# Performance work log

Measured on AMD Instinct MI355X. Metric: run time of the kernel, lower is better.

Reference implementation:

```python
import jax, jax.numpy as jnp
import numpy as np

C = 128
N_SRC = 50000
N_MID = 50000
N_DST = 50000
E1 = 640000
E2 = 640000


def setup_inputs() -> dict:
    key = jax.random.key(0)
    ks = jax.random.split(key, 16)
    def lin(k):
        kw, kb = jax.random.split(k)
        bound = 1.0 / np.sqrt(C)
        W = jax.random.uniform(kw, (C, C), jnp.float32, -bound, bound)
        b = jax.random.uniform(kb, (C,), jnp.float32, -bound, bound)
        return W, b
    W1_w, W1_b = lin(ks[0])
    W2_w, W2_b = lin(ks[1])
    q_w, q_b = lin(ks[2])
    k_w, k_b = lin(ks[3])
    v_w, v_b = lin(ks[4])
    return {
        'x_src': jax.random.normal(ks[5], (N_SRC, C), jnp.float32),
        'x_mid': jax.random.normal(ks[6], (N_MID, C), jnp.float32),
        'x_dst': jax.random.normal(ks[7], (N_DST, C), jnp.float32),
        'edge_index_1': jax.random.randint(ks[8], (2, E1), 0, N_MID, jnp.int64),
        'edge_index_2': jax.random.randint(ks[9], (2, E2), 0, N_DST, jnp.int64),
        'W1_w': W1_w, 'W1_b': W1_b,
        'W2_w': W2_w, 'W2_b': W2_b,
        'q_w': q_w, 'q_b': q_b,
        'k_w': k_w, 'k_b': k_b,
        'v_w': v_w, 'v_b': v_b,
    }


def reference(x_src, x_mid, x_dst, edge_index_1, edge_index_2,
              W1_w, W1_b, W2_w, W2_b, q_w, q_b, k_w, k_b, v_w, v_b):
    src_idx_1, mid_idx_1 = edge_index_1[0], edge_index_1[1]
    # gather + small per-edge linear fuse: [E1, C]
    h_fuse = (x_mid[mid_idx_1] @ W1_w.T + W1_b) + (x_src[src_idx_1] @ W2_w.T + W2_b)
    # scatter-add into mid nodes: [N_mid, C]
    h_mid_agg = jax.ops.segment_sum(h_fuse, mid_idx_1, num_segments=x_mid.shape[0])
    mid_idx_2, dst_idx_2 = edge_index_2[0], edge_index_2[1]
    h_mid_g = h_mid_agg[mid_idx_2]          # [E2, C]
    k = h_mid_g @ k_w.T + k_b               # [E2, C]
    v = h_mid_g @ v_w.T + v_b               # [E2, C]
    q = x_dst[dst_idx_2] @ q_w.T + q_b      # [E2, C]
    scale = jnp.float32(C) ** 0.5
    # NOTE: faithful to the original: softmax is GLOBAL over all edges (dim=0)
    alpha = jax.nn.softmax((q * k).sum(-1) / scale, axis=0)  # [E2]
    msg = v * alpha[:, None]
    msg_dst = jax.ops.segment_sum(msg, dst_idx_2, num_segments=x_dst.shape[0])
    return msg_dst
```

## Files before the change

### kernel.cpp

```cpp
#include <hip/hip_runtime.h>
#include <cstdint>
#include <cstddef>


using f16   = _Float16;
using f16x2 = __attribute__((ext_vector_type(2))) _Float16;
using f16x4 = __attribute__((ext_vector_type(4))) _Float16;
using f16x8 = __attribute__((ext_vector_type(8))) _Float16;
using f32x4 = __attribute__((ext_vector_type(4))) float;

#define SP_CHUNK 2048

__device__ __forceinline__ int swzv(int v) { return v ^ ((v >> 4) & 7); }

__global__ __launch_bounds__(256) void conv_weights(
    const float* __restrict__ W1, const float* __restrict__ W2,
    const float* __restrict__ vw, const float* __restrict__ b1,
    const float* __restrict__ b2, f16* __restrict__ wh,
    float* __restrict__ b12)
{
    int idx = blockIdx.x * 256 + threadIdx.x;
    if (idx < 3 * 16384) {
        const float* src = (idx < 16384) ? W1 :
                           (idx < 2 * 16384) ? W2 : vw;
        wh[idx] = (f16)src[idx & 16383];
    } else if (idx < 3 * 16384 + 128) {
        int j = idx - 3 * 16384;
        b12[j] = b1[j] + b2[j];
    }
}

__global__ __launch_bounds__(256) void prep_qk(
    const float* __restrict__ qw, const float* __restrict__ kw,
    const float* __restrict__ qb, const float* __restrict__ kb,
    f16* __restrict__ wqk, float* __restrict__ bqk,
    float* __restrict__ wqkb, float* __restrict__ cconst)
{
    int e = blockIdx.x * 256 + threadIdx.x;
    int col = e >> 7, i = e & 127;
    float s = 0.f;
    for (int j = 0; j < 128; ++j)
        s += qw[j * 128 + i] * kw[j * 128 + col];
    wqk[col * 128 + i] = (f16)s;
    if (blockIdx.x == 0) {
        int t = threadIdx.x;
        if (t < 128) {
            float s1 = 0.f, s2 = 0.f;
            for (int j = 0; j < 128; ++j) {
                s1 += qw[j * 128 + t] * kb[j];
                s2 += qb[j] * kw[j * 128 + t];
            }
            wqkb[t] = s1;
            bqk[t] = s2;
        } else if (t == 128) {
            float s3 = 0.f;
            for (int j = 0; j < 128; ++j) s3 += qb[j] * kb[j];
            cconst[0] = s3;
        }
    }
}

__global__ __launch_bounds__(256) void conv3_f16(
    const float* __restrict__ xa, f16* __restrict__ ya, int na4,
    const float* __restrict__ xb, f16* __restrict__ yb, int nb4,
    const float* __restrict__ xc, f16* __restrict__ yc, int nc4)
{
    int j = blockIdx.x * 256 + threadIdx.x;
    const float* x; f16* y;
    if (j < na4) { x = xa; y = ya; }
    else {
        j -= na4;
        if (j < nb4) { x = xb; y = yb; }
        else {
            j -= nb4;
            if (j >= nc4) return;
            x = xc; y = yc;
        }
    }
    float4 v = ((const float4*)x)[j];
    f16x4 o = {(f16)v.x, (f16)v.y, (f16)v.z, (f16)v.w};
    ((f16x4*)y)[j] = o;
}

__global__ __launch_bounds__(256) void coarse_hist(
    const int* __restrict__ k1, int E1, int nb1, int* __restrict__ ch1p,
    const int* __restrict__ k2, int E2, int nb2, int* __restrict__ ch2p)
{
    __shared__ int h[512];
    int tid = threadIdx.x;
    for (int i = tid; i < nb1 + nb2; i += 256) h[i] = 0;
    __syncthreads();
    int stride = gridDim.x * 256;
    for (int e = blockIdx.x * 256 + tid; e < E1; e += stride)
        atomicAdd(&h[k1[e] >> 8], 1);
    for (int e = blockIdx.x * 256 + tid; e < E2; e += stride)
        atomicAdd(&h[nb1 + (k2[e] >> 8)], 1);
    __syncthreads();
    for (int i = tid; i < nb1; i += 256) { int c = h[i];        if (c) atomicAdd(&ch1p[i * 16], c); }
    for (int i = tid; i < nb2; i += 256) { int c = h[nb1 + i];  if (c) atomicAdd(&ch2p[i * 16], c); }
}

__global__ __launch_bounds__(256) void coarse_scan(
    const int* __restrict__ ch1p, int nb1, int E1, int* __restrict__ cb1, int* __restrict__ cur1p,
    const int* __restrict__ ch2p, int nb2, int E2, int* __restrict__ cb2, int* __restrict__ cur2p)
{
    __shared__ int sd[256];
    int tid = threadIdx.x;
    int v = (tid < nb1) ? ch1p[tid * 16] : 0;
    sd[tid] = v; __syncthreads();
    for (int d = 1; d < 256; d <<= 1) {
        int t = (tid >= d) ? sd[tid - d] : 0;
        __syncthreads(); sd[tid] += t; __syncthreads();
    }
    if (tid < nb1) { int ex = sd[tid] - v; cb1[tid] = ex; cur1p[tid * 16] = ex; }
    if (tid == 0) cb1[nb1] = E1;
    __syncthreads();
    int v2 = (tid < nb2) ? ch2p[tid * 16] : 0;
    sd[tid] = v2; __syncthreads();
    for (int d = 1; d < 256; d <<= 1) {
        int t = (tid >= d) ? sd[tid - d] : 0;
        __syncthreads(); sd[tid] += t; __syncthreads();
    }
    if (tid < nb2) { int ex = sd[tid] - v2; cb2[tid] = ex; cur2p[tid * 16] = ex; }
    if (tid == 0) cb2[nb2] = E2;
}

__device__ __forceinline__ void scatter_chunk(
    const int* __restrict__ keys, const int* __restrict__ pay, int E,
    int* __restrict__ curp, int2* __restrict__ out,
    int* hist, int* base, int nbk, int chunk)
{
    int tid = threadIdx.x;
    int start = chunk * SP_CHUNK;
    if (start >= E) return;
    int end = start + SP_CHUNK; if (end > E) end = E;

    for (int i = tid; i < nbk; i += 256) hist[i] = 0;
    __syncthreads();
    for (int i = start + tid; i < end; i += 256)
        atomicAdd(&hist[keys[i] >> 8], 1);
    __syncthreads();
    for (int i = tid; i < nbk; i += 256) {
        int c = hist[i];
        base[i] = c ? atomicAdd(&curp[i * 16], c) : 0;
        hist[i] = 0;
    }
    __syncthreads();
    for (int i = start + tid; i < end; i += 256) {
        int key = keys[i];
        int b = key >> 8;
        int lp = atomicAdd(&hist[b], 1);
        out[base[b] + lp] = make_int2(key, pay[i]);
    }
}

__global__ __launch_bounds__(256) void scatter_pairs_blk(
    const int* __restrict__ ei1, int E1, int nb1, int* __restrict__ cur1p,
    int2* __restrict__ p1, int nch1,
    const int* __restrict__ ei2, int E2, int nb2, int* __restrict__ cur2p,
    int2* __restrict__ p2)
{
    __shared__ int hist[256];
    __shared__ int base[256];
    int b = blockIdx.x;
    if (b < nch1)
        scatter_chunk(ei1 + E1, ei1, E1, cur1p, p1, hist, base, nb1, b);
    else
        scatter_chunk(ei2 + E2, ei2, E2, cur2p, p2, hist, base, nb2, b - nch1);
}

__global__ __launch_bounds__(256) void bucket_sort(
    const int2* __restrict__ p1, const int* __restrict__ cb1, int nb1, int N1, int E1,
    int* __restrict__ off1, int* __restrict__ out1,
    const int2* __restrict__ p2, const int* __restrict__ cb2, int nb2, int N2, int E2,
    int* __restrict__ off2, int* __restrict__ out2)
{
    __shared__ int hist[256];
    __shared__ int scn[256];
    int kb = blockIdx.x;
    const int2* pairs; const int* cb; int N, E; int* offk; int* outp;
    if (kb < nb1) { pairs = p1; cb = cb1; N = N1; E = E1; offk = off1; outp = out1; }
    else { kb -= nb1; pairs = p2; cb = cb2; N = N2; E = E2; offk = off2; outp = out2; }
    int tid = threadIdx.x;
    int base = cb[kb], cnt = cb[kb + 1] - base;
    int key0 = kb << 8;
    int nk = N - key0; if (nk > 256) nk = 256;

    hist[tid] = 0;
    __syncthreads();
    for (int i = tid; i < cnt; i += 256)
        atomicAdd(&hist[pairs[base + i].x - key0], 1);
    __syncthreads();
    int v = hist[tid];
    scn[tid] = v; __syncthreads();
    for (int d = 1; d < 256; d <<= 1) {
        int t = (tid >= d) ? scn[tid - d] : 0;
        __syncthreads(); scn[tid] += t; __syncthreads();
    }
    int ex = scn[tid] - v;
    if (tid < nk) offk[key0 + tid] = base + ex;
    if (tid == 0 && key0 + nk == N) offk[N] = E;
    hist[tid] = ex;
    __syncthreads();
    for (int i = tid; i < cnt; i += 256) {
        int2 pr = pairs[base + i];
        int p = atomicAdd(&hist[pr.x - key0], 1);
        outp[base + p] = pr.y;
    }
}

__global__ __launch_bounds__(256) void pull1_h(
    const f16* __restrict__ xs, const int* __restrict__ off,
    const int* __restrict__ lst, f16* __restrict__ s,
    float* __restrict__ deg, int N)
{
    int w = blockIdx.x * 4 + (threadIdx.x >> 6);
    int l = threadIdx.x & 63;
    if (w >= N) return;
    int b = off[w], e = off[w + 1];
    float ax = 0.f, ay = 0.f;
    for (int i = b; i < e; i += 16) {
        int idx[16];
        f16x2 a[16];
#pragma unroll
        for (int u = 0; u < 16; ++u) {
            int id = i + u;
            idx[u] = lst[(id < e) ? id : b];
        }
#pragma unroll
        for (int u = 0; u < 16; ++u)
            a[u] = *(const f16x2*)(xs + (size_t)idx[u] * 128 + l * 2);
#pragma unroll
        for (int u = 0; u < 16; ++u) {
            bool val = (i + u) < e;
            ax += val ? (float)a[u][0] : 0.f;
            ay += val ? (float)a[u][1] : 0.f;
        }
    }
    f16x2 o = {(f16)ax, (f16)ay};
    *(f16x2*)(s + (size_t)w * 128 + l * 2) = o;
    if (l == 0) deg[w] = (float)(e - b);
}

__global__ __launch_bounds__(256) void gemm_stage1_mfma(
    const f16* Xm, const f16* S, const f16* __restrict__ w12,
    const float* __restrict__ b12, const float* __restrict__ deg,
    f16* H, int M)
{
    __shared__ f16 lw[32768];
    int tid = threadIdx.x;
    int lane = tid & 63;
    int r16 = lane & 15, quad = lane >> 4;
    int gw = (blockIdx.x * 256 + tid) >> 6;
    int mb = gw * 16;
    bool active = mb < M;
    int row = mb + r16; if (row >= M) row = M - 1;

    f16x8 a1[4], a2[4];
    if (active) {
        const f16* xa = Xm + (size_t)row * 128 + quad * 8;
        const f16* xb = S  + (size_t)row * 128 + quad * 8;
#pragma unroll
        for (int kb = 0; kb < 4; ++kb) {
            a1[kb] = *(const f16x8*)(xa + kb * 32);
            a2[kb] = *(const f16x8*)(xb + kb * 32);
        }
    }
    {
        const f16x8* gsrc = (const f16x8*)w12;
        f16x8* ldst = (f16x8*)lw;
#pragma unroll
        for (int u = 0; u < 16; ++u) {
            int i = u * 256 + tid;
            ldst[swzv(i)] = gsrc[i];
        }
    }
    __syncthreads();
    if (!active) return;

    f32x4 accA[8], accB[8];
#pragma unroll
    for (int t = 0; t < 8; ++t) {
        accA[t] = (f32x4){0.f, 0.f, 0.f, 0.f};
        accB[t] = (f32x4){0.f, 0.f, 0.f, 0.f};
    }
    const f16x8* lv = (const f16x8*)lw;
#pragma unroll
    for (int kb = 0; kb < 4; ++kb) {
#pragma unroll
        for (int t = 0; t < 8; ++t) {
            int r = t * 16 + r16;
            f16x8 bw1 = lv[swzv(r * 16 + kb * 4 + quad)];
            f16x8 bw2 = lv[swzv((r + 128) * 16 + kb * 4 + quad)];
            accA[t] = __builtin_amdgcn_mfma_f32_16x16x32_f16(a1[kb], bw1, accA[t], 0, 0, 0);
            accB[t] = __builtin_amdgcn_mfma_f32_16x16x32_f16(a2[kb], bw2, accB[t], 0, 0, 0);
        }
    }
    float dv[4];
#pragma unroll
    for (int i = 0; i < 4; ++i) {
        int r = mb + quad * 4 + i;
        dv[i] = (r < M) ? deg[r] : 0.f;
    }
#pragma unroll
    for (int t = 0; t < 8; ++t) {
        int col = t * 16 + r16;
        float bb = b12[col];
#pragma unroll
        for (int i = 0; i < 4; ++i) {
            int r = mb + quad * 4 + i;
            if (r < M)
                H[(size_t)r * 128 + col] = (f16)(dv[i] * (accA[t][i] + bb) + accB[t][i]);
        }
    }
}

__global__ __launch_bounds__(256) void gemm_qp_mfma(
    const f16* X, const f16* __restrict__ W,
    const float* __restrict__ bias, const float* __restrict__ wqkb,
    const float* __restrict__ cconst, f16* Y, float* __restrict__ qc, int M)
{
    __shared__ f16 lw[16384];
    int tid = threadIdx.x;
    int lane = tid & 63;
    int r16 = lane & 15, quad = lane >> 4;
    int gw = (blockIdx.x * 256 + tid) >> 6;
    int mb = gw * 16;
    bool active = mb < M;
    int row = mb + r16; if (row >= M) row = M - 1;

    f16x8 a[4];
    if (active) {
        const f16* xp = X + (size_t)row * 128 + quad * 8;
#pragma unroll
        for (int kb = 0; kb < 4; ++kb)
            a[kb] = *(const f16x8*)(xp + kb * 32);
    }
    {
        const f16x8* gsrc = (const f16x8*)W;
        f16x8* ldst = (f16x8*)lw;
#pragma unroll
        for (int u = 0; u < 8; ++u) {
            int i = u * 256 + tid;
            ldst[swzv(i)] = gsrc[i];
        }
    }
    __syncthreads();
    if (!active) return;

    f32x4 acc[8];
#pragma unroll
    for (int t = 0; t < 8; ++t) acc[t] = (f32x4){0.f, 0.f, 0.f, 0.f};

    float pq = 0.f;
    const f16x8* lv = (const f16x8*)lw;
#pragma unroll
    for (int kb = 0; kb < 4; ++kb) {
#pragma unroll
        for (int j = 0; j < 8; ++j)
            pq += (float)a[kb][j] * wqkb[kb * 32 + quad * 8 + j];
#pragma unroll
        for (int t = 0; t < 8; ++t) {
            f16x8 b = lv[swzv((t * 16 + r16) * 16 + kb * 4 + quad)];
            acc[t] = __builtin_amdgcn_mfma_f32_16x16x32_f16(a[kb], b, acc[t], 0, 0, 0);
        }
    }
    pq += __shfl_xor(pq, 16);
    pq += __shfl_xor(pq, 32);
    if (quad == 0 && mb + r16 < M) qc[mb + r16] = pq + cconst[0];
#pragma unroll
    for (int t = 0; t < 8; ++t) {
        int col = t * 16 + r16;
        float bv = bias[col];
#pragma unroll
        for (int i = 0; i < 4; ++i) {
            int r = mb + quad * 4 + i;
            if (r < M) Y[(size_t)r * 128 + col] = (f16)(acc[t][i] + bv);
        }
    }
}

__global__ __launch_bounds__(256) void gemm_v_mfma(
    const f16* U, const f16* __restrict__ W,
    const float* __restrict__ vb, const float* __restrict__ sexp,
    const float* __restrict__ S, float* __restrict__ out, int M)
{
    __shared__ f16 lw[16384];
    int tid = threadIdx.x;
    int lane = tid & 63;
    int r16 = lane & 15, quad = lane >> 4;
    int gw = (blockIdx.x * 256 + tid) >> 6;
    int mb = gw * 16;
    bool active = mb < M;
    int row = mb + r16; if (row >= M) row = M - 1;

    f16x8 a[4];
    if (active) {
        const f16* xp = U + (size_t)row * 128 + quad * 8;
#pragma unroll
        for (int kb = 0; kb < 4; ++kb)
            a[kb] = *(const f16x8*)(xp + kb * 32);
    }
    {
        const f16x8* gsrc = (const f16x8*)W;
        f16x8* ldst = (f16x8*)lw;
#pragma unroll
        for (int u = 0; u < 8; ++u) {
            int i = u * 256 + tid;
            ldst[swzv(i)] = gsrc[i];
        }
    }
    __syncthreads();
    if (!active) return;

    f32x4 acc[8];
#pragma unroll
    for (int t = 0; t < 8; ++t) acc[t] = (f32x4){0.f, 0.f, 0.f, 0.f};

    const f16x8* lv = (const f16x8*)lw;
#pragma unroll
    for (int kb = 0; kb < 4; ++kb) {
#pragma unroll
        for (int t = 0; t < 8; ++t) {
            f16x8 b = lv[swzv((t * 16 + r16) * 16 + kb * 4 + quad)];
            acc[t] = __builtin_amdgcn_mfma_f32_16x16x32_f16(a[kb], b, acc[t], 0, 0, 0);
        }
    }
    float invS = 1.0f / S[0];
    float sv[4];
#pragma unroll
    for (int i = 0; i < 4; ++i) {
        int r = mb + quad * 4 + i;
        sv[i] = (r < M) ? sexp[r] * invS : 0.f;
    }
#pragma unroll
    for (int t = 0; t < 8; ++t) {
        int col = t * 16 + r16;
        float bv = vb[col];
#pragma unroll
        for (int i = 0; i < 4; ++i) {
            int r = mb + quad * 4 + i;
            if (r < M)
                out[(size_t)r * 128 + col] = (acc[t][i] + bv) * sv[i];
        }
    }
}

__global__ __launch_bounds__(256) void attn_fused_h(
    const f16* __restrict__ Qp, const f16* __restrict__ H,
    const float* __restrict__ qc, const int* __restrict__ off,
    const int* __restrict__ lstm, f16* __restrict__ U,
    float* __restrict__ sexp, float* __restrict__ partial, int N)
{
    const int tid  = threadIdx.x;
    const int w    = blockIdx.x * 4 + (tid >> 6);
    const int lane = tid & 63;
    const int sub  = lane >> 4;
    const int c    = lane & 15;
    const float scale = 0.08838834764831845f;

    float acc[8];
#pragma unroll
    for (int j = 0; j < 8; ++j) acc[j] = 0.f;
    float ssum = 0.f;
    float factor = 0.f;

    if (w < N) {
        factor = __expf(qc[w] * scale);
        int b = off[w], e = off[w + 1];
        if (b < e) {
            f16x8 qh = *(const f16x8*)(Qp + (size_t)w * 128 + c * 8);
            f16x2 q2[4];
#pragma unroll
            for (int j = 0; j < 4; ++j) q2[j] = ((const f16x2*)&qh)[j];
            for (int i = b; i < e; i += 16) {
                int m[4]; bool val[4];
#pragma unroll
                for (int u = 0; u < 4; ++u) {
                    int id = i + sub * 4 + u;
                    val[u] = id < e;
                    m[u] = lstm[val[u] ? id : b];
                }
                f16x8 hh[4];
#pragma unroll
                for (int u = 0; u < 4; ++u)
                    hh[u] = *(const f16x8*)(H + (size_t)m[u] * 128 + c * 8);
                float p[4];
#pragma unroll
                for (int u = 0; u < 4; ++u) {
                    float s = 0.f;
                    const f16x2* h2 = (const f16x2*)&hh[u];
#pragma unroll
                    for (int j = 0; j < 4; ++j)
#if __has_builtin(__builtin_amdgcn_fdot2)
                        s = __builtin_amdgcn_fdot2(q2[j], h2[j], s, false);
#else
                        s += (float)q2[j][0] * (float)h2[j][0]
                           + (float)q2[j][1] * (float)h2[j][1];
#endif
                    p[u] = s;
                }
#pragma unroll
                for (int o = 1; o < 16; o <<= 1) {
#pragma unroll
                    for (int u = 0; u < 4; ++u)
                        p[u] += __shfl_xor(p[u], o);
                }
                float a[4];
#pragma unroll
                for (int u = 0; u < 4; ++u)
                    a[u] = val[u] ? __expf(p[u] * scale) : 0.f;
                ssum += (a[0] + a[1]) + (a[2] + a[3]);
#pragma unroll
                for (int u = 0; u < 4; ++u)
#pragma unroll
                    for (int j = 0; j < 8; ++j)
                        acc[j] += a[u] * (float)hh[u][j];
            }
        }
    }
    float stot = ssum;
    stot += __shfl_xor(stot, 16);
    stot += __shfl_xor(stot, 32);

    if (w < N) {
#pragma unroll
        for (int j = 0; j < 8; ++j) {
            acc[j] += __shfl_xor(acc[j], 16);
            acc[j] += __shfl_xor(acc[j], 32);
        }
        if (sub == 0) {
            float inv = (stot > 0.f) ? 1.0f / stot : 0.f;
            f16x8 o;
#pragma unroll
            for (int j = 0; j < 8; ++j) o[j] = (f16)(acc[j] * inv);
            *(f16x8*)(U + (size_t)w * 128 + c * 8) = o;
        }
    }
    float sg = stot * factor;
    if (lane == 0 && w < N) sexp[w] = sg;
    __shared__ float bs[4];
    if (lane == 0) bs[tid >> 6] = sg;
    __syncthreads();
    if (tid == 0) partial[blockIdx.x] = bs[0] + bs[1] + bs[2] + bs[3];
}

__global__ __launch_bounds__(256) void reduce_partials(
    const float* __restrict__ partial, float* __restrict__ S, int n)
{
    float v = 0.f;
    for (int i = threadIdx.x; i < n; i += 256) v += partial[i];
#pragma unroll
    for (int o = 32; o; o >>= 1) v += __shfl_down(v, o, 64);
    __shared__ float ws[4];
    if ((threadIdx.x & 63) == 0) ws[threadIdx.x >> 6] = v;
    __syncthreads();
    if (threadIdx.x == 0) S[0] = ws[0] + ws[1] + ws[2] + ws[3];
}

extern "C" void kernel_launch(void* const* d_in, const int* in_sizes, int n_in,
                              void* d_out, int out_size, void* d_ws, size_t ws_size,
                              hipStream_t stream)
{
    const float* x_src = (const float*)d_in[0];
    const float* x_mid = (const float*)d_in[1];
    const float* x_dst = (const float*)d_in[2];
    const int*   ei1   = (const int*)d_in[3];
    const int*   ei2   = (const int*)d_in[4];
    const float* W1_w  = (const float*)d_in[5];
    const float* W1_b  = (const float*)d_in[6];
    const float* W2_w  = (const float*)d_in[7];
    const float* W2_b  = (const float*)d_in[8];
    const float* q_w   = (const float*)d_in[9];
    const float* q_b   = (const float*)d_in[10];
    const float* k_w   = (const float*)d_in[11];
    const float* k_b   = (const float*)d_in[12];
    const float* v_w   = (const float*)d_in[13];
    const float* v_b   = (const float*)d_in[14];

    const int NSRC = in_sizes[0] / 128;
    const int NMID = in_sizes[1] / 128;
    const int NDST = in_sizes[2] / 128;
    const int E1   = in_sizes[3] / 2;
    const int E2   = in_sizes[4] / 2;
    const int nb2g = (NDST + 3) / 4;
    const int nb1  = (NMID + 255) >> 8;
    const int nb2  = (NDST + 255) >> 8;

    auto al4 = [](size_t n) { return (n + 3) & ~(size_t)3; };

    f16* xs_h = (f16*)d_ws;
    f16* xm_h = xs_h + (size_t)NSRC * 128;
    f16* xd_h = xm_h + (size_t)NMID * 128;
    f16* s_h  = xd_h + (size_t)NDST * 128;
    f16* qp_h = s_h  + (size_t)NMID * 128;
    f16* u_h  = qp_h + (size_t)NDST * 128;
    f16* w_h  = u_h  + (size_t)NDST * 128;
    f16* w1h = w_h, *w2h = w_h + 16384, *wvh = w_h + 2 * 16384;
    f16* wqk = w_h + 3 * 16384;

    float* b12 = (float*)(w_h + 4 * 16384);
    float* bqk = b12 + 128;
    float* wqkb = bqk + 128;
    float* cconst = wqkb + 128;
    float* deg = cconst + 4;
    float* qcv = deg + al4(NMID);
    float* sexp = qcv + al4(NDST);
    float* partial = sexp + al4(NDST);
    float* scal = partial + al4(nb2g);

    int2* pairs1 = (int2*)(scal + 16);
    int2* pairs2 = pairs1 + E1;
    int*  cb1   = (int*)(pairs2 + E2);
    int*  cb2   = cb1 + al4(nb1 + 1);
    int*  ch1p  = cb2 + al4(nb2 + 1);
    int*  ch2p  = ch1p + nb1 * 16;
    int*  cur1p = ch2p + nb2 * 16;
    int*  cur2p = cur1p + nb1 * 16;
    int*  off1  = cur2p + nb2 * 16;
    int*  off2  = off1 + al4(NMID + 1);
    int*  lst1  = off2 + al4(NDST + 1);
    int*  lstm2 = lst1 + al4(E1);

    hipMemsetAsync(ch1p, 0, (size_t)(nb1 + nb2) * 16 * sizeof(int), stream);

    conv_weights<<<(3 * 16384 + 128 + 255) / 256, 256, 0, stream>>>(
        W1_w, W2_w, v_w, W1_b, W2_b, w_h, b12);
    prep_qk<<<64, 256, 0, stream>>>(q_w, k_w, q_b, k_b, wqk, bqk, wqkb, cconst);
    {
        int na4 = NSRC * 32, nb4 = NMID * 32, nc4 = NDST * 32;
        conv3_f16<<<(na4 + nb4 + nc4 + 255) / 256, 256, 0, stream>>>(
            x_src, xs_h, na4, x_mid, xm_h, nb4, x_dst, xd_h, nc4);
    }

    coarse_hist<<<512, 256, 0, stream>>>(ei1 + E1, E1, nb1, ch1p,
                                         ei2 + E2, E2, nb2, ch2p);
    coarse_scan<<<1, 256, 0, stream>>>(ch1p, nb1, E1, cb1, cur1p,
                                       ch2p, nb2, E2, cb2, cur2p);
    {
        int nch1 = (E1 + SP_CHUNK - 1) / SP_CHUNK;
        int nch2 = (E2 + SP_CHUNK - 1) / SP_CHUNK;
        scatter_pairs_blk<<<nch1 + nch2, 256, 0, stream>>>(
            ei1, E1, nb1, cur1p, pairs1, nch1,
            ei2, E2, nb2, cur2p, pairs2);
    }
    bucket_sort<<<nb1 + nb2, 256, 0, stream>>>(
        pairs1, cb1, nb1, NMID, E1, off1, lst1,
        pairs2, cb2, nb2, NDST, E2, off2, lstm2);

    pull1_h<<<(NMID + 3) / 4, 256, 0, stream>>>(xs_h, off1, lst1, s_h, deg, NMID);

    int gbm = ((NMID + 15) / 16 + 3) / 4;
    gemm_stage1_mfma<<<gbm, 256, 0, stream>>>(xm_h, s_h, w_h , b12, deg,
                                              xm_h , NMID);
    int gbd = ((NDST + 15) / 16 + 3) / 4;
    gemm_qp_mfma<<<gbd, 256, 0, stream>>>(xd_h, wqk, bqk, wqkb, cconst,
                                          qp_h, qcv, NDST);

    attn_fused_h<<<nb2g, 256, 0, stream>>>(qp_h, xm_h, qcv, off2, lstm2,
                                           u_h, sexp, partial, NDST);
    reduce_partials<<<1, 256, 0, stream>>>(partial, scal, nb2g);
    gemm_v_mfma<<<gbd, 256, 0, stream>>>(u_h, wvh, v_b, sexp, scal,
                                         (float*)d_out, NDST);
}
```

Before: 344.3 us.

## Fuse setup kernels, read fp32 inputs directly in GEMMs, replace partial reduce with atomics

Merges weight conversion, the QK weight precompute and the x_src fp16 conversion into one setup kernel. The x_mid and x_dst fp16 copies are dropped, and the stage-1 and q-projection GEMMs now load fp32 rows and convert them in registers. The separate reduce_partials kernel is replaced by a per-block atomicAdd into a global sum that coarse_scan zeroes. This removes kernel launches and one round of activation writes and reads, at the cost of wider fp32 loads and float atomics whose summation order is nondeterministic.

```diff
diff --git a/kernel.cpp b/kernel.cpp
--- a/kernel.cpp
+++ b/kernel.cpp
@@ -13,11 +13,15 @@
 
 __device__ __forceinline__ int swzv(int v) { return v ^ ((v >> 4) & 7); }
 
-__global__ __launch_bounds__(256) void conv_weights(
+__global__ __launch_bounds__(256) void setup_all(
     const float* __restrict__ W1, const float* __restrict__ W2,
     const float* __restrict__ vw, const float* __restrict__ b1,
-    const float* __restrict__ b2, f16* __restrict__ wh,
-    float* __restrict__ b12)
+    const float* __restrict__ b2, const float* __restrict__ qw,
+    const float* __restrict__ kw, const float* __restrict__ qb,
+    const float* __restrict__ kb, const float* __restrict__ xsrc,
+    f16* __restrict__ wh, float* __restrict__ b12,
+    float* __restrict__ bqk, float* __restrict__ wqkb,
+    float* __restrict__ cconst, f16* __restrict__ xs_h, int na4)
 {
     int idx = blockIdx.x * 256 + threadIdx.x;
     if (idx < 3 * 16384) {
@@ -27,59 +31,34 @@
     } else if (idx < 3 * 16384 + 128) {
         int j = idx - 3 * 16384;
         b12[j] = b1[j] + b2[j];
-    }
-}
-
-__global__ __launch_bounds__(256) void prep_qk(
-    const float* __restrict__ qw, const float* __restrict__ kw,
-    const float* __restrict__ qb, const float* __restrict__ kb,
-    f16* __restrict__ wqk, float* __restrict__ bqk,
-    float* __restrict__ wqkb, float* __restrict__ cconst)
-{
-    int e = blockIdx.x * 256 + threadIdx.x;
-    int col = e >> 7, i = e & 127;
-    float s = 0.f;
-    for (int j = 0; j < 128; ++j)
-        s += qw[j * 128 + i] * kw[j * 128 + col];
-    wqk[col * 128 + i] = (f16)s;
-    if (blockIdx.x == 0) {
-        int t = threadIdx.x;
-        if (t < 128) {
-            float s1 = 0.f, s2 = 0.f;
-            for (int j = 0; j < 128; ++j) {
-                s1 += qw[j * 128 + t] * kb[j];
-                s2 += qb[j] * kw[j * 128 + t];
-            }
-            wqkb[t] = s1;
-            bqk[t] = s2;
-        } else if (t == 128) {
-            float s3 = 0.f;
-            for (int j = 0; j < 128; ++j) s3 += qb[j] * kb[j];
-            cconst[0] = s3;
-        }
-    }
-}
-
-__global__ __launch_bounds__(256) void conv3_f16(
-    const float* __restrict__ xa, f16* __restrict__ ya, int na4,
-    const float* __restrict__ xb, f16* __restrict__ yb, int nb4,
-    const float* __restrict__ xc, f16* __restrict__ yc, int nc4)
-{
-    int j = blockIdx.x * 256 + threadIdx.x;
-    const float* x; f16* y;
-    if (j < na4) { x = xa; y = ya; }
-    else {
-        j -= na4;
-        if (j < nb4) { x = xb; y = yb; }
-        else {
-            j -= nb4;
-            if (j >= nc4) return;
-            x = xc; y = yc;
-        }
-    }
-    float4 v = ((const float4*)x)[j];
-    f16x4 o = {(f16)v.x, (f16)v.y, (f16)v.z, (f16)v.w};
-    ((f16x4*)y)[j] = o;
+    } else if (idx < 4 * 16384 + 128) {
+        int e = idx - (3 * 16384 + 128);
+        int col = e >> 7, i = e & 127;
+        float s = 0.f;
+        for (int j = 0; j < 128; ++j)
+            s += qw[j * 128 + i] * kw[j * 128 + col];
+        wh[3 * 16384 + col * 128 + i] = (f16)s;
+    } else if (idx < 4 * 16384 + 256) {
+        int t = idx - (4 * 16384 + 128);
+        float s1 = 0.f, s2 = 0.f;
+        for (int j = 0; j < 128; ++j) {
+            s1 += qw[j * 128 + t] * kb[j];
+            s2 += qb[j] * kw[j * 128 + t];
+        }
+        wqkb[t] = s1;
+        bqk[t] = s2;
+    } else if (idx == 4 * 16384 + 256) {
+        float s3 = 0.f;
+        for (int j = 0; j < 128; ++j) s3 += qb[j] * kb[j];
+        cconst[0] = s3;
+    } else {
+        int j = idx - (4 * 16384 + 257);
+        if (j < na4) {
+            float4 v = ((const float4*)xsrc)[j];
+            f16x4 o = {(f16)v.x, (f16)v.y, (f16)v.z, (f16)v.w};
+            ((f16x4*)xs_h)[j] = o;
+        }
+    }
 }
 
 __global__ __launch_bounds__(256) void coarse_hist(
@@ -102,10 +81,12 @@
 
 __global__ __launch_bounds__(256) void coarse_scan(
     const int* __restrict__ ch1p, int nb1, int E1, int* __restrict__ cb1, int* __restrict__ cur1p,
-    const int* __restrict__ ch2p, int nb2, int E2, int* __restrict__ cb2, int* __restrict__ cur2p)
+    const int* __restrict__ ch2p, int nb2, int E2, int* __restrict__ cb2, int* __restrict__ cur2p,
+    float* __restrict__ Sg)
 {
     __shared__ int sd[256];
     int tid = threadIdx.x;
+    if (tid == 0) Sg[0] = 0.f;
     int v = (tid < nb1) ? ch1p[tid * 16] : 0;
     sd[tid] = v; __syncthreads();
     for (int d = 1; d < 256; d <<= 1) {
@@ -243,9 +224,9 @@
 }
 
 __global__ __launch_bounds__(256) void gemm_stage1_mfma(
-    const f16* Xm, const f16* S, const f16* __restrict__ w12,
-    const float* __restrict__ b12, const float* __restrict__ deg,
-    f16* H, int M)
+    const float* __restrict__ Xm, const f16* __restrict__ S,
+    const f16* __restrict__ w12, const float* __restrict__ b12,
+    const float* __restrict__ deg, f16* __restrict__ H, int M)
 {
     __shared__ f16 lw[32768];
     int tid = threadIdx.x;
@@ -256,13 +237,15 @@
     bool active = mb < M;
     int row = mb + r16; if (row >= M) row = M - 1;
 
-    f16x8 a1[4], a2[4];
+    f32x4 alo[4], ahi[4];
+    f16x8 a2[4];
     if (active) {
-        const f16* xa = Xm + (size_t)row * 128 + quad * 8;
-        const f16* xb = S  + (size_t)row * 128 + quad * 8;
+        const float* xa = Xm + (size_t)row * 128 + quad * 8;
+        const f16* xb = S + (size_t)row * 128 + quad * 8;
 #pragma unroll
         for (int kb = 0; kb < 4; ++kb) {
-            a1[kb] = *(const f16x8*)(xa + kb * 32);
+            alo[kb] = *(const f32x4*)(xa + kb * 32);
+            ahi[kb] = *(const f32x4*)(xa + kb * 32 + 4);
             a2[kb] = *(const f16x8*)(xb + kb * 32);
         }
     }
@@ -277,6 +260,15 @@
     }
     __syncthreads();
     if (!active) return;
+
+    f16x8 a1[4];
+#pragma unroll
+    for (int kb = 0; kb < 4; ++kb)
+#pragma unroll
+        for (int j = 0; j < 4; ++j) {
+            a1[kb][j] = (f16)alo[kb][j];
+            a1[kb][4 + j] = (f16)ahi[kb][j];
+        }
 
     f32x4 accA[8], accB[8];
 #pragma unroll
@@ -316,9 +308,10 @@
 }
 
 __global__ __launch_bounds__(256) void gemm_qp_mfma(
-    const f16* X, const f16* __restrict__ W,
+    const float* __restrict__ Xd, const f16* __restrict__ W,
     const float* __restrict__ bias, const float* __restrict__ wqkb,
-    const float* __restrict__ cconst, f16* Y, float* __restrict__ qc, int M)
+    const float* __restrict__ cconst, f16* __restrict__ Qp,
+    float* __restrict__ qc, int M)
 {
     __shared__ f16 lw[16384];
     int tid = threadIdx.x;
@@ -329,12 +322,14 @@
     bool active = mb < M;
     int row = mb + r16; if (row >= M) row = M - 1;
 
-    f16x8 a[4];
+    f32x4 alo[4], ahi[4];
     if (active) {
-        const f16* xp = X + (size_t)row * 128 + quad * 8;
-#pragma unroll
-        for (int kb = 0; kb < 4; ++kb)
-            a[kb] = *(const f16x8*)(xp + kb * 32);
+        const float* xp = Xd + (size_t)row * 128 + quad * 8;
+#pragma unroll
+        for (int kb = 0; kb < 4; ++kb) {
+            alo[kb] = *(const f32x4*)(xp + kb * 32);
+            ahi[kb] = *(const f32x4*)(xp + kb * 32 + 4);
+        }
     }
     {
         const f16x8* gsrc = (const f16x8*)W;
@@ -348,17 +343,24 @@
     __syncthreads();
     if (!active) return;
 
+    f16x8 a[4];
+    float pq = 0.f;
+#pragma unroll
+    for (int kb = 0; kb < 4; ++kb)
+#pragma unroll
+        for (int j = 0; j < 4; ++j) {
+            a[kb][j] = (f16)alo[kb][j];
+            a[kb][4 + j] = (f16)ahi[kb][j];
+            pq += alo[kb][j] * wqkb[kb * 32 + quad * 8 + j];
+            pq += ahi[kb][j] * wqkb[kb * 32 + quad * 8 + 4 + j];
+        }
+
     f32x4 acc[8];
 #pragma unroll
     for (int t = 0; t < 8; ++t) acc[t] = (f32x4){0.f, 0.f, 0.f, 0.f};
-
-    float pq = 0.f;
     const f16x8* lv = (const f16x8*)lw;
 #pragma unroll
     for (int kb = 0; kb < 4; ++kb) {
-#pragma unroll
-        for (int j = 0; j < 8; ++j)
-            pq += (float)a[kb][j] * wqkb[kb * 32 + quad * 8 + j];
 #pragma unroll
         for (int t = 0; t < 8; ++t) {
             f16x8 b = lv[swzv((t * 16 + r16) * 16 + kb * 4 + quad)];
@@ -375,7 +377,7 @@
 #pragma unroll
         for (int i = 0; i < 4; ++i) {
             int r = mb + quad * 4 + i;
-            if (r < M) Y[(size_t)r * 128 + col] = (f16)(acc[t][i] + bv);
+            if (r < M) Qp[(size_t)r * 128 + col] = (f16)(acc[t][i] + bv);
         }
     }
 }
@@ -450,7 +452,7 @@
     const f16* __restrict__ Qp, const f16* __restrict__ H,
     const float* __restrict__ qc, const int* __restrict__ off,
     const int* __restrict__ lstm, f16* __restrict__ U,
-    float* __restrict__ sexp, float* __restrict__ partial, int N)
+    float* __restrict__ sexp, float* __restrict__ Sg, int N)
 {
     const int tid  = threadIdx.x;
     const int w    = blockIdx.x * 4 + (tid >> 6);
@@ -542,20 +544,10 @@
     __shared__ float bs[4];
     if (lane == 0) bs[tid >> 6] = sg;
     __syncthreads();
-    if (tid == 0) partial[blockIdx.x] = bs[0] + bs[1] + bs[2] + bs[3];
-}
-
-__global__ __launch_bounds__(256) void reduce_partials(
-    const float* __restrict__ partial, float* __restrict__ S, int n)
-{
-    float v = 0.f;
-    for (int i = threadIdx.x; i < n; i += 256) v += partial[i];
-#pragma unroll
-    for (int o = 32; o; o >>= 1) v += __shfl_down(v, o, 64);
-    __shared__ float ws[4];
-    if ((threadIdx.x & 63) == 0) ws[threadIdx.x >> 6] = v;
-    __syncthreads();
-    if (threadIdx.x == 0) S[0] = ws[0] + ws[1] + ws[2] + ws[3];
+    if (tid == 0) {
+        float t = bs[0] + bs[1] + bs[2] + bs[3];
+        if (t != 0.f) atomicAdd(Sg, t);
+    }
 }
 
 extern "C" void kernel_launch(void* const* d_in, const int* in_sizes, int n_in,
@@ -590,13 +582,12 @@
     auto al4 = [](size_t n) { return (n + 3) & ~(size_t)3; };
 
     f16* xs_h = (f16*)d_ws;
-    f16* xm_h = xs_h + (size_t)NSRC * 128;
-    f16* xd_h = xm_h + (size_t)NMID * 128;
-    f16* s_h  = xd_h + (size_t)NDST * 128;
-    f16* qp_h = s_h  + (size_t)NMID * 128;
+    f16* h_h  = xs_h + (size_t)NSRC * 128;
+    f16* s_h  = h_h + (size_t)NMID * 128;
+    f16* qp_h = s_h + (size_t)NMID * 128;
     f16* u_h  = qp_h + (size_t)NDST * 128;
-    f16* w_h  = u_h  + (size_t)NDST * 128;
-    f16* w1h = w_h, *w2h = w_h + 16384, *wvh = w_h + 2 * 16384;
+    f16* w_h  = u_h + (size_t)NDST * 128;
+    f16* wvh = w_h + 2 * 16384;
     f16* wqk = w_h + 3 * 16384;
 
     float* b12 = (float*)(w_h + 4 * 16384);
@@ -606,8 +597,7 @@
     float* deg = cconst + 4;
     float* qcv = deg + al4(NMID);
     float* sexp = qcv + al4(NDST);
-    float* partial = sexp + al4(NDST);
-    float* scal = partial + al4(nb2g);
+    float* scal = sexp + al4(NDST);
 
     int2* pairs1 = (int2*)(scal + 16);
     int2* pairs2 = pairs1 + E1;
@@ -624,19 +614,18 @@
 
     hipMemsetAsync(ch1p, 0, (size_t)(nb1 + nb2) * 16 * sizeof(int), stream);
 
-    conv_weights<<<(3 * 16384 + 128 + 255) / 256, 256, 0, stream>>>(
-        W1_w, W2_w, v_w, W1_b, W2_b, w_h, b12);
-    prep_qk<<<64, 256, 0, stream>>>(q_w, k_w, q_b, k_b, wqk, bqk, wqkb, cconst);
     {
-        int na4 = NSRC * 32, nb4 = NMID * 32, nc4 = NDST * 32;
-        conv3_f16<<<(na4 + nb4 + nc4 + 255) / 256, 256, 0, stream>>>(
-            x_src, xs_h, na4, x_mid, xm_h, nb4, x_dst, xd_h, nc4);
+        int na4 = NSRC * 32;
+        int total = 4 * 16384 + 257 + na4;
+        setup_all<<<(total + 255) / 256, 256, 0, stream>>>(
+            W1_w, W2_w, v_w, W1_b, W2_b, q_w, k_w, q_b, k_b, x_src,
+            w_h, b12, bqk, wqkb, cconst, xs_h, na4);
     }
 
     coarse_hist<<<512, 256, 0, stream>>>(ei1 + E1, E1, nb1, ch1p,
                                          ei2 + E2, E2, nb2, ch2p);
     coarse_scan<<<1, 256, 0, stream>>>(ch1p, nb1, E1, cb1, cur1p,
-                                       ch2p, nb2, E2, cb2, cur2p);
+                                       ch2p, nb2, E2, cb2, cur2p, scal);
     {
         int nch1 = (E1 + SP_CHUNK - 1) / SP_CHUNK;
         int nch2 = (E2 + SP_CHUNK - 1) / SP_CHUNK;
@@ -651,15 +640,14 @@
     pull1_h<<<(NMID + 3) / 4, 256, 0, stream>>>(xs_h, off1, lst1, s_h, deg, NMID);
 
     int gbm = ((NMID + 15) / 16 + 3) / 4;
-    gemm_stage1_mfma<<<gbm, 256, 0, stream>>>(xm_h, s_h, w_h , b12, deg,
-                                              xm_h , NMID);
     int gbd = ((NDST + 15) / 16 + 3) / 4;
-    gemm_qp_mfma<<<gbd, 256, 0, stream>>>(xd_h, wqk, bqk, wqkb, cconst,
+    gemm_stage1_mfma<<<gbm, 256, 0, stream>>>(x_mid, s_h, w_h , b12,
+                                              deg, h_h, NMID);
+    gemm_qp_mfma<<<gbd, 256, 0, stream>>>(x_dst, wqk, bqk, wqkb, cconst,
                                           qp_h, qcv, NDST);
 
-    attn_fused_h<<<nb2g, 256, 0, stream>>>(qp_h, xm_h, qcv, off2, lstm2,
-                                           u_h, sexp, partial, NDST);
-    reduce_partials<<<1, 256, 0, stream>>>(partial, scal, nb2g);
+    attn_fused_h<<<nb2g, 256, 0, stream>>>(qp_h, h_h, qcv, off2, lstm2,
+                                           u_h, sexp, scal, NDST);
     gemm_v_mfma<<<gbd, 256, 0, stream>>>(u_h, wvh, v_b, sexp, scal,
                                          (float*)d_out, NDST);
 }
```

After: 445.2 us. 29.3% more time.
